# Performance work log

Measured on AMD Instinct MI355X. Metric: run time of the kernel, lower is better.

Reference implementation:

```python
import jax, jax.numpy as jnp
import numpy as np

N_NODES = 100000
N_EDGES = 3200000
D_FEAT = 64


def setup_inputs() -> dict:
    key = jax.random.key(0)
    k1, k2, k3 = jax.random.split(key, 3)
    inputs = jax.random.normal(k1, (N_NODES, D_FEAT), dtype=jnp.float32)
    rows = jax.random.randint(k2, (N_EDGES,), 0, N_NODES, dtype=jnp.int32)
    cols = jax.random.randint(k3, (N_EDGES,), 0, N_NODES, dtype=jnp.int32)
    return {"inputs": inputs, "rows": rows, "cols": cols}


def reference(inputs, rows, cols):
    # adj is a binary sparse [N, N] matrix given as COO edges (rows[e], cols[e]) -> 1.0
    n = inputs.shape[0]
    # degrees = adj.sum(dim=1): count of outgoing edges per row
    deg = jax.ops.segment_sum(jnp.ones_like(rows, dtype=inputs.dtype), rows,
                              num_segments=n)  # [N]
    # degrees + (degrees == 0): avoid div-by-zero for isolated nodes
    deg = deg + (deg == 0).astype(inputs.dtype)
    # spmm(adj, inputs): sum neighbor features into each row
    agg = jax.ops.segment_sum(inputs[cols], rows, num_segments=n)  # [N, d]
    return agg / deg[:, None]
```

## Files before the change

### kernel.cpp

```cpp
#include <hip/hip_runtime.h>
#include <hip/hip_bf16.h>
#include <hip/hip_fp16.h>

#define D_FEAT 64
#define TILE_EDGES 8192
#define SC_THREADS 512
#define ROWS_PER_BUK 128
#define BUK_SHIFT 7
#define STRIDE 4480

#define HALF_ROWS 64
#define LCOL_SZ 2560

__global__ void __launch_bounds__(SC_THREADS) scatter_kernel(
    const float* __restrict__ x, __half* __restrict__ x16,
    const int* __restrict__ rows, const int* __restrict__ cols,
    int* __restrict__ gcount, int* __restrict__ ebuf,
    int n_edges, int nbuk, int n4)
{
    __shared__ int lh[1024];
    __shared__ int lscan[1024];
    __shared__ int lgb[1024];
    __shared__ int lsort[TILE_EDGES];

    const int t = threadIdx.x;

    {
        const int per = (n4 + gridDim.x - 1) / gridDim.x;
        const int s0 = blockIdx.x * per;
        const int e0 = min(s0 + per, n4);
        for (int i = s0 + t; i < e0; i += SC_THREADS) {
            float4 v = ((const float4*)x)[i];
            ushort4 u;
            u.x = __half_as_ushort(__float2half(v.x));
            u.y = __half_as_ushort(__float2half(v.y));
            u.z = __half_as_ushort(__float2half(v.z));
            u.w = __half_as_ushort(__float2half(v.w));
            ((ushort4*)x16)[i] = u;
        }
    }

    lh[t] = 0; lh[t + 512] = 0;
    __syncthreads();

    const int tb = blockIdx.x * TILE_EDGES;
    const int te = min(tb + TILE_EDGES, n_edges);

    for (int e = tb + t * 4; e < te; e += SC_THREADS * 4) {
        if (e + 4 <= te) {
            int4 r4 = *(const int4*)&rows[e];
            atomicAdd(&lh[r4.x >> BUK_SHIFT], 1);
            atomicAdd(&lh[r4.y >> BUK_SHIFT], 1);
            atomicAdd(&lh[r4.z >> BUK_SHIFT], 1);
            atomicAdd(&lh[r4.w >> BUK_SHIFT], 1);
        } else {
            for (int k = e; k < te; ++k) atomicAdd(&lh[rows[k] >> BUK_SHIFT], 1);
        }
    }
    __syncthreads();

    const int c0 = lh[2 * t], c1 = lh[2 * t + 1];
    const int s2 = c0 + c1;
    lscan[t] = s2;
    __syncthreads();
    for (int ofs = 1; ofs < 512; ofs <<= 1) {
        int val = lscan[t];
        int add = (t >= ofs) ? lscan[t - ofs] : 0;
        __syncthreads();
        lscan[t] = val + add;
        __syncthreads();
    }
    const int excl = lscan[t] - s2;
    __syncthreads();
    lscan[2 * t] = excl;
    lscan[2 * t + 1] = excl + c0;
    lgb[2 * t]     = c0 ? atomicAdd(&gcount[2 * t], c0) : 0;
    lgb[2 * t + 1] = c1 ? atomicAdd(&gcount[2 * t + 1], c1) : 0;
    lh[2 * t] = excl;
    lh[2 * t + 1] = excl + c0;
    __syncthreads();

    for (int e = tb + t * 4; e < te; e += SC_THREADS * 4) {
        if (e + 4 <= te) {
            int4 r4 = *(const int4*)&rows[e];
            int4 c4 = *(const int4*)&cols[e];
            int p0 = atomicAdd(&lh[r4.x >> BUK_SHIFT], 1);
            int p1 = atomicAdd(&lh[r4.y >> BUK_SHIFT], 1);
            int p2 = atomicAdd(&lh[r4.z >> BUK_SHIFT], 1);
            int p3 = atomicAdd(&lh[r4.w >> BUK_SHIFT], 1);
            lsort[p0] = ((r4.x & (ROWS_PER_BUK - 1)) << 17) | c4.x;
            lsort[p1] = ((r4.y & (ROWS_PER_BUK - 1)) << 17) | c4.y;
            lsort[p2] = ((r4.z & (ROWS_PER_BUK - 1)) << 17) | c4.z;
            lsort[p3] = ((r4.w & (ROWS_PER_BUK - 1)) << 17) | c4.w;
        } else {
            for (int k = e; k < te; ++k) {
                int r = rows[k], c = cols[k];
                int pos = atomicAdd(&lh[r >> BUK_SHIFT], 1);
                lsort[pos] = ((r & (ROWS_PER_BUK - 1)) << 17) | c;
            }
        }
    }
    __syncthreads();

    const int hw = t >> 5;
    const int hl = t & 31;
    for (int b = hw; b < nbuk; b += 16) {
        const int ls = lscan[b];
        const int cnt = lh[b] - ls;
        const int gb = lgb[b];
        for (int i = hl; i < cnt; i += 32) {
            int gpos = gb + i;
            if (gpos < STRIDE) ebuf[b * STRIDE + gpos] = lsort[ls + i];
        }
    }
}

__global__ void __launch_bounds__(256) gather_kernel(
    const uint4* __restrict__ x4, const int* __restrict__ gcount,
    const int* __restrict__ ebuf, float* __restrict__ out, int n_nodes)
{
    __shared__ int lcol[LCOL_SZ];
    __shared__ int lh[HALF_ROWS];
    __shared__ int lscan[HALF_ROWS];
    __shared__ int lcur[HALF_ROWS];
    const int bb = blockIdx.x;
    const int b = bb >> 1;
    const int half = bb & 1;
    const int t = threadIdx.x;

    const int start = b * STRIDE;
    int cnt = gcount[b];
    if (cnt > STRIDE) cnt = STRIDE;

    if (t < HALF_ROWS) lh[t] = 0;
    __syncthreads();
    for (int i = t; i < cnt; i += 256) {
        int p = ebuf[start + i];
        int r = p >> 17;
        if ((r >> 6) == half) atomicAdd(&lh[r & (HALF_ROWS - 1)], 1);
    }
    __syncthreads();

    if (t < 64) {
        int c = lh[t];
        int val = c;
        #pragma unroll
        for (int ofs = 1; ofs < 64; ofs <<= 1) {
            int n = __shfl_up(val, ofs, 64);
            if (t >= ofs) val += n;
        }
        int excl = val - c;
        lscan[t] = excl;
        lcur[t] = excl;
    }
    __syncthreads();

    for (int i = t; i < cnt; i += 256) {
        int p = ebuf[start + i];
        int r = p >> 17;
        if ((r >> 6) == half) {
            int pos = atomicAdd(&lcur[r & (HALF_ROWS - 1)], 1);
            if (pos < LCOL_SZ) lcol[pos] = p & 0x1FFFF;
        }
    }
    __syncthreads();

    const int w = t >> 6;
    const int lane = t & 63;
    const int eg = lane >> 3;
    const int g2 = lane & 7;

    union U { uint4 u; __half2 h2[4]; };

    for (int rr = 0; rr < 16; ++rr) {
        const int r = w * 16 + rr;
        const int row = (b << BUK_SHIFT) + (half << 6) + r;
        const int s = lscan[r];
        const int d = lh[r];
        int e = s + d;
        if (e > LCOL_SZ) e = LCOL_SZ;

        const __half2 z = __float2half2_rn(0.0f);
        __half2 h[4];
        #pragma unroll
        for (int k = 0; k < 4; ++k) h[k] = z;

        int j = s;
        for (; j + 32 <= e; j += 32) {
            int cA = lcol[j + eg], cB = lcol[j + 8 + eg];
            int cC = lcol[j + 16 + eg], cD = lcol[j + 24 + eg];
            U A, B, C, D;
            A.u = x4[cA * 8 + g2];
            B.u = x4[cB * 8 + g2];
            C.u = x4[cC * 8 + g2];
            D.u = x4[cD * 8 + g2];
            #pragma unroll
            for (int k = 0; k < 4; ++k)
                h[k] = __hadd2(h[k], __hadd2(__hadd2(A.h2[k], B.h2[k]),
                                             __hadd2(C.h2[k], D.h2[k])));
        }
        for (; j + 16 <= e; j += 16) {
            int cA = lcol[j + eg], cB = lcol[j + 8 + eg];
            U A, B;
            A.u = x4[cA * 8 + g2];
            B.u = x4[cB * 8 + g2];
            #pragma unroll
            for (int k = 0; k < 4; ++k)
                h[k] = __hadd2(h[k], __hadd2(A.h2[k], B.h2[k]));
        }
        for (; j + 8 <= e; j += 8) {
            int c = lcol[j + eg];
            U A;
            A.u = x4[c * 8 + g2];
            #pragma unroll
            for (int k = 0; k < 4; ++k) h[k] = __hadd2(h[k], A.h2[k]);
        }
        int rem = e - j;
        if (eg < rem) {
            int c = lcol[j + eg];
            U A;
            A.u = x4[c * 8 + g2];
            #pragma unroll
            for (int k = 0; k < 4; ++k) h[k] = __hadd2(h[k], A.h2[k]);
        }

        float a[8];
        #pragma unroll
        for (int k = 0; k < 4; ++k) {
            float2 f = __half22float2(h[k]);
            a[2 * k] = f.x;
            a[2 * k + 1] = f.y;
        }
        #pragma unroll
        for (int k = 0; k < 8; ++k) {
            a[k] += __shfl_down(a[k], 8, 64);
            a[k] += __shfl_down(a[k], 16, 64);
            a[k] += __shfl_down(a[k], 32, 64);
        }

        if (eg == 0 && row < n_nodes) {
            const float inv = 1.0f / (float)(d > 0 ? d : 1);
            float4* o = (float4*)(out + ((long)row << 6) + (g2 << 3));
            o[0] = make_float4(a[0] * inv, a[1] * inv, a[2] * inv, a[3] * inv);
            o[1] = make_float4(a[4] * inv, a[5] * inv, a[6] * inv, a[7] * inv);
        }
    }
}

extern "C" void kernel_launch(void* const* d_in, const int* in_sizes, int n_in,
                              void* d_out, int out_size, void* d_ws, size_t ws_size,
                              hipStream_t stream) {
    const float* x  = (const float*)d_in[0];
    const int* rows = (const int*)d_in[1];
    const int* cols = (const int*)d_in[2];
    float* out = (float*)d_out;

    const int n_nodes = in_sizes[0] / D_FEAT;
    const int n_edges = in_sizes[1];
    const int n_feat_total = in_sizes[0];
    const int n4 = n_feat_total / 4;

    const int nbuk   = (n_nodes + ROWS_PER_BUK - 1) >> BUK_SHIFT;
    const int ntiles = (n_edges + TILE_EDGES - 1) / TILE_EDGES;

    __half* x16 = (__half*)d_ws;
    int* gcount = (int*)(x16 + n_feat_total);
    int* ebuf   = gcount + nbuk;

    hipMemsetAsync(gcount, 0, (size_t)nbuk * sizeof(int), stream);

    scatter_kernel<<<ntiles, SC_THREADS, 0, stream>>>(
        x, x16, rows, cols, gcount, ebuf, n_edges, nbuk, n4);

    gather_kernel<<<nbuk * 2, 256, 0, stream>>>((const uint4*)x16, gcount, ebuf, out, n_nodes);
}
```

Baseline: 182.1 us.

## Split fp16 feature table into four column groups and gather per group

The fp16 copy of the features is now stored as four column-group planes of 16 features (32 bytes per node each). The gather walks each row's edge list four times, once per plane, loading one 4-byte half2 per lane and accumulating in fp32 instead of fp16. The aim is a smaller working set per pass so the gathered plane stays in cache, plus better accuracy, at the cost of re-reading the column lists four times and issuing four times as many small loads.

```diff
diff --git a/kernel.cpp b/kernel.cpp
--- a/kernel.cpp
+++ b/kernel.cpp
@@ -11,6 +11,8 @@
 
 #define HALF_ROWS 64
 #define LCOL_SZ 2560
+#define NGRP 4
+
 
 __global__ void __launch_bounds__(SC_THREADS) scatter_kernel(
     const float* __restrict__ x, __half* __restrict__ x16,
@@ -29,6 +31,7 @@
         const int per = (n4 + gridDim.x - 1) / gridDim.x;
         const int s0 = blockIdx.x * per;
         const int e0 = min(s0 + per, n4);
+        const int ng4 = n4 >> 2;
         for (int i = s0 + t; i < e0; i += SC_THREADS) {
             float4 v = ((const float4*)x)[i];
             ushort4 u;
@@ -36,7 +39,11 @@
             u.y = __half_as_ushort(__float2half(v.y));
             u.z = __half_as_ushort(__float2half(v.z));
             u.w = __half_as_ushort(__float2half(v.w));
-            ((ushort4*)x16)[i] = u;
+            const int n  = i >> 4;
+            const int f4 = i & 15;
+            const int g  = f4 >> 2;
+            const int dst = g * ng4 + (n << 2) + (f4 & 3);
+            ((ushort4*)x16)[dst] = u;
         }
     }
 
@@ -116,8 +123,8 @@
 }
 
 __global__ void __launch_bounds__(256) gather_kernel(
-    const uint4* __restrict__ x4, const int* __restrict__ gcount,
-    const int* __restrict__ ebuf, float* __restrict__ out, int n_nodes)
+    const unsigned int* __restrict__ x1t, const int* __restrict__ gcount,
+    const int* __restrict__ ebuf, float* __restrict__ out, int n_nodes, int gs)
 {
     __shared__ int lcol[LCOL_SZ];
     __shared__ int lh[HALF_ROWS];
@@ -170,80 +177,63 @@
     const int eg = lane >> 3;
     const int g2 = lane & 7;
 
-    union U { uint4 u; __half2 h2[4]; };
-
-    for (int rr = 0; rr < 16; ++rr) {
-        const int r = w * 16 + rr;
-        const int row = (b << BUK_SHIFT) + (half << 6) + r;
-        const int s = lscan[r];
-        const int d = lh[r];
-        int e = s + d;
-        if (e > LCOL_SZ) e = LCOL_SZ;
-
-        const __half2 z = __float2half2_rn(0.0f);
-        __half2 h[4];
-        #pragma unroll
-        for (int k = 0; k < 4; ++k) h[k] = z;
-
-        int j = s;
-        for (; j + 32 <= e; j += 32) {
-            int cA = lcol[j + eg], cB = lcol[j + 8 + eg];
-            int cC = lcol[j + 16 + eg], cD = lcol[j + 24 + eg];
-            U A, B, C, D;
-            A.u = x4[cA * 8 + g2];
-            B.u = x4[cB * 8 + g2];
-            C.u = x4[cC * 8 + g2];
-            D.u = x4[cD * 8 + g2];
-            #pragma unroll
-            for (int k = 0; k < 4; ++k)
-                h[k] = __hadd2(h[k], __hadd2(__hadd2(A.h2[k], B.h2[k]),
-                                             __hadd2(C.h2[k], D.h2[k])));
-        }
-        for (; j + 16 <= e; j += 16) {
-            int cA = lcol[j + eg], cB = lcol[j + 8 + eg];
-            U A, B;
-            A.u = x4[cA * 8 + g2];
-            B.u = x4[cB * 8 + g2];
-            #pragma unroll
-            for (int k = 0; k < 4; ++k)
-                h[k] = __hadd2(h[k], __hadd2(A.h2[k], B.h2[k]));
-        }
-        for (; j + 8 <= e; j += 8) {
-            int c = lcol[j + eg];
-            U A;
-            A.u = x4[c * 8 + g2];
-            #pragma unroll
-            for (int k = 0; k < 4; ++k) h[k] = __hadd2(h[k], A.h2[k]);
-        }
-        int rem = e - j;
-        if (eg < rem) {
-            int c = lcol[j + eg];
-            U A;
-            A.u = x4[c * 8 + g2];
-            #pragma unroll
-            for (int k = 0; k < 4; ++k) h[k] = __hadd2(h[k], A.h2[k]);
-        }
-
-        float a[8];
-        #pragma unroll
-        for (int k = 0; k < 4; ++k) {
-            float2 f = __half22float2(h[k]);
-            a[2 * k] = f.x;
-            a[2 * k + 1] = f.y;
-        }
-        #pragma unroll
-        for (int k = 0; k < 8; ++k) {
-            a[k] += __shfl_down(a[k], 8, 64);
-            a[k] += __shfl_down(a[k], 16, 64);
-            a[k] += __shfl_down(a[k], 32, 64);
-        }
-
-        if (eg == 0 && row < n_nodes) {
-            const float inv = 1.0f / (float)(d > 0 ? d : 1);
-            float4* o = (float4*)(out + ((long)row << 6) + (g2 << 3));
-            o[0] = make_float4(a[0] * inv, a[1] * inv, a[2] * inv, a[3] * inv);
-            o[1] = make_float4(a[4] * inv, a[5] * inv, a[6] * inv, a[7] * inv);
-        }
+    for (int g = 0; g < NGRP; ++g) {
+        const int gb_ = g * gs;
+        for (int rr = 0; rr < 16; ++rr) {
+            const int r = w * 16 + rr;
+            const int row = (b << BUK_SHIFT) + (half << 6) + r;
+            const int s = lscan[r];
+            const int d = lh[r];
+            int e = s + d;
+            if (e > LCOL_SZ) e = LCOL_SZ;
+
+            float a0 = 0.0f, a1 = 0.0f;
+
+            int j = s;
+            for (; j + 32 <= e; j += 32) {
+                int cA = lcol[j + eg],      cB = lcol[j + 8 + eg];
+                int cC = lcol[j + 16 + eg], cD = lcol[j + 24 + eg];
+                unsigned int uA = x1t[gb_ + cA * 8 + g2];
+                unsigned int uB = x1t[gb_ + cB * 8 + g2];
+                unsigned int uC = x1t[gb_ + cC * 8 + g2];
+                unsigned int uD = x1t[gb_ + cD * 8 + g2];
+                float2 fA = __half22float2(*reinterpret_cast<const __half2*>(&uA));
+                float2 fB = __half22float2(*reinterpret_cast<const __half2*>(&uB));
+                float2 fC = __half22float2(*reinterpret_cast<const __half2*>(&uC));
+                float2 fD = __half22float2(*reinterpret_cast<const __half2*>(&uD));
+                a0 += (fA.x + fB.x) + (fC.x + fD.x);
+                a1 += (fA.y + fB.y) + (fC.y + fD.y);
+            }
+            for (; j + 8 <= e; j += 8) {
+                int c = lcol[j + eg];
+                unsigned int u = x1t[gb_ + c * 8 + g2];
+                float2 f = __half22float2(*reinterpret_cast<const __half2*>(&u));
+                a0 += f.x;
+                a1 += f.y;
+            }
+            int rem = e - j;
+            if (eg < rem) {
+                int c = lcol[j + eg];
+                unsigned int u = x1t[gb_ + c * 8 + g2];
+                float2 f = __half22float2(*reinterpret_cast<const __half2*>(&u));
+                a0 += f.x;
+                a1 += f.y;
+            }
+
+            a0 += __shfl_down(a0, 8, 64);
+            a0 += __shfl_down(a0, 16, 64);
+            a0 += __shfl_down(a0, 32, 64);
+            a1 += __shfl_down(a1, 8, 64);
+            a1 += __shfl_down(a1, 16, 64);
+            a1 += __shfl_down(a1, 32, 64);
+
+            if (eg == 0 && row < n_nodes) {
+                const float inv = 1.0f / (float)(d > 0 ? d : 1);
+                float2* o = (float2*)(out + ((long)row << 6) + (g << 4) + (g2 << 1));
+                *o = make_float2(a0 * inv, a1 * inv);
+            }
+        }
+        __syncthreads();
     }
 }
 
@@ -272,5 +262,7 @@
     scatter_kernel<<<ntiles, SC_THREADS, 0, stream>>>(
         x, x16, rows, cols, gcount, ebuf, n_edges, nbuk, n4);
 
-    gather_kernel<<<nbuk * 2, 256, 0, stream>>>((const uint4*)x16, gcount, ebuf, out, n_nodes);
+    const int gs = n_nodes * 8;
+    gather_kernel<<<nbuk * 2, 256, 0, stream>>>(
+        (const unsigned int*)x16, gcount, ebuf, out, n_nodes, gs);
 }
```

Result: slower. 230.5 us (+26.6%).
